# Performance work log

Hardware: AMD Instinct MI355X
Metric: run time of the kernel (lower is better)

Reference implementation:

```python
import jax, jax.numpy as jnp
import numpy as np

N_NODES = 40000
N_EDGES = 640000
N_GRAPHS = 64
D_IN = 128
D_H = 128
N_LAYERS = 3
EPS = 1e-5


def _layer_norm(x, g, b):
    mu = jnp.mean(x, axis=-1, keepdims=True)
    var = jnp.var(x, axis=-1, keepdims=True)
    return (x - mu) * jax.lax.rsqrt(var + EPS) * g + b


def _sage_conv(x, src, dst, Wl, bl, Wr):
    # mean aggregation of neighbor messages: i <- mean_{j: (j->i)} x_j
    msg = x[src]                                              # [E, d]
    agg = jax.ops.segment_sum(msg, dst, num_segments=N_NODES)  # [N, d]
    deg = jax.ops.segment_sum(jnp.ones((src.shape[0],), x.dtype), dst,
                              num_segments=N_NODES)
    agg = agg / jnp.clip(deg, 1.0)[:, None]
    # out = lin_l(agg) + lin_r(x)
    return agg @ Wl.T + bl + x @ Wr.T


def setup_inputs() -> dict:
    key = jax.random.key(0)
    ks = jax.random.split(key, 12)
    s = 0.05
    x = jax.random.normal(ks[0], (N_NODES, D_IN), jnp.float32)
    edge_index = jax.random.randint(ks[1], (2, N_EDGES), 0, N_NODES, jnp.int64)
    batch = jnp.sort(jax.random.randint(ks[2], (N_NODES,), 0, N_GRAPHS, jnp.int64))
    fc_w = jax.random.normal(ks[3], (D_H, D_IN), jnp.float32) * s
    fc_b = jax.random.normal(ks[4], (D_H,), jnp.float32) * s
    Wl = jax.random.normal(ks[5], (N_LAYERS, D_H, D_H), jnp.float32) * s
    bl = jax.random.normal(ks[6], (N_LAYERS, D_H), jnp.float32) * s
    Wr = jax.random.normal(ks[7], (N_LAYERS, D_H, D_H), jnp.float32) * s
    ln_g = jnp.ones((N_LAYERS - 1, D_H), jnp.float32)
    ln_b = jnp.zeros((N_LAYERS - 1, D_H), jnp.float32)
    return {"x": x, "edge_index": edge_index, "batch": batch,
            "fc_w": fc_w, "fc_b": fc_b, "Wl": Wl, "bl": bl, "Wr": Wr,
            "ln_g": ln_g, "ln_b": ln_b}


def reference(x, edge_index, batch, fc_w, fc_b, Wl, bl, Wr, ln_g, ln_b):
    src, dst = edge_index[0], edge_index[1]
    # input projection + ReLU
    h = jax.nn.relu(x @ fc_w.T + fc_b)
    # GraphSAGE stack: norm + ReLU between layers, none after the last
    for i in range(N_LAYERS):
        h = _sage_conv(h, src, dst, Wl[i], bl[i], Wr[i])
        if i < N_LAYERS - 1:
            h = jax.nn.relu(_layer_norm(h, ln_g[i], ln_b[i]))
    node_embed = h                                            # [N, D_H]
    graph_embed = jax.ops.segment_sum(node_embed, batch,
                                      num_segments=N_GRAPHS)  # [G, D_H]
    return node_embed, graph_embed
```

## Files before the change

kernel.cpp:

```cpp
#include <hip/hip_runtime.h>
#include <hip/hip_bf16.h>


#define N_NODES 40000
#define N_EDGES 640000
#define N_GRAPHS 64
#define D 128
#define NODE_ELEMS 5120000
#define N_TILES 1250
#define ELL_W 64
#define ZERO_INTS 48192

typedef __hip_bfloat16 bf16;
typedef __attribute__((ext_vector_type(8))) short bf16x8;
typedef __attribute__((ext_vector_type(4))) float f32x4;

__device__ __forceinline__ float b2f(bf16 v) { return __bfloat162float(v); }
__device__ __forceinline__ bf16 f2b(float v) { return __float2bfloat16(v); }
__device__ __forceinline__ float lo2f(unsigned w) { return __uint_as_float(w << 16); }
__device__ __forceinline__ float hi2f(unsigned w) { return __uint_as_float(w & 0xffff0000u); }
__device__ __forceinline__ unsigned packbf(float a, float b) {
    union { bf16 h[2]; unsigned u; } c;
    c.h[0] = f2b(a); c.h[1] = f2b(b);
    return c.u;
}
__device__ __forceinline__ int is_bf16(const unsigned* lng) {
    return (lng[0] == 0x3f803f80u) ? 1 : 0;
}
__device__ __forceinline__ int edge_is_i64(const void* edge) {
    const unsigned* ew = (const unsigned*)edge;
    return (ew[1] == 0u && ew[3] == 0u && ew[5] == 0u) ? 1 : 0;
}

union U8 { uint4 u; bf16x8 s; };

__device__ __forceinline__ bf16x8 load8(const void* base, long idx, int isb) {
    if (isb) {
        U8 t;
        t.u = *(const uint4*)((const bf16*)base + idx);
        return t.s;
    }
    const float* f = (const float*)base + idx;
    float4 f0 = *(const float4*)f;
    float4 f1 = *(const float4*)(f + 4);
    union { bf16 h[8]; bf16x8 s; } t;
    t.h[0] = f2b(f0.x); t.h[1] = f2b(f0.y); t.h[2] = f2b(f0.z); t.h[3] = f2b(f0.w);
    t.h[4] = f2b(f1.x); t.h[5] = f2b(f1.y); t.h[6] = f2b(f1.z); t.h[7] = f2b(f1.w);
    return t.s;
}

__global__ __launch_bounds__(256, 2) void k_gemm0(
    const void* __restrict__ X, const void* __restrict__ fcw,
    const void* __restrict__ fcb, bf16* __restrict__ outb,
    int* __restrict__ zbase, const unsigned* __restrict__ lngraw) {
    for (int i = blockIdx.x * 256 + threadIdx.x; i < ZERO_INTS; i += gridDim.x * 256)
        zbase[i] = 0;

    const int tid = threadIdx.x;
    const int lane = tid & 63;
    const int wave = tid >> 6;
    const int n = lane & 15, q = lane >> 4;
    const int rowgrp = wave >> 1;
    const int cb = (wave & 1) * 64;
    const int isb = is_bf16(lngraw);

    bf16x8 wf[4][4];
#pragma unroll
    for (int ct = 0; ct < 4; ct++)
#pragma unroll
        for (int ks = 0; ks < 4; ks++)
            wf[ct][ks] = load8(fcw, (long)(cb + ct * 16 + n) * 128 + ks * 32 + q * 8, isb);
    float bz[4];
#pragma unroll
    for (int ct = 0; ct < 4; ct++)
        bz[ct] = isb ? b2f(((const bf16*)fcb)[cb + ct * 16 + n])
                     : ((const float*)fcb)[cb + ct * 16 + n];

    const f32x4 zero = {0.f, 0.f, 0.f, 0.f};
    for (int tile = blockIdx.x; tile < N_TILES; tile += gridDim.x) {
        const long rbase = (long)tile * 32 + rowgrp * 16 + n;
        f32x4 acc[4] = {zero, zero, zero, zero};
        bf16x8 af[4];
#pragma unroll
        for (int ks = 0; ks < 4; ks++)
            af[ks] = load8(X, rbase * 128 + ks * 32 + q * 8, isb);
#pragma unroll
        for (int ct = 0; ct < 4; ct++)
#pragma unroll
            for (int ks = 0; ks < 4; ks++)
                acc[ct] = __builtin_amdgcn_mfma_f32_16x16x32_bf16(
                    af[ks], wf[ct][ks], acc[ct], 0, 0, 0);
#pragma unroll
        for (int ct = 0; ct < 4; ct++) {
            const int col = cb + ct * 16 + n;
#pragma unroll
            for (int r = 0; r < 4; r++) {
                const long row = (long)tile * 32 + rowgrp * 16 + q * 4 + r;
                outb[row * 128 + col] = f2b(fmaxf(acc[ct][r] + bz[ct], 0.f));
            }
        }
    }
}

#define CW2_TOTAL 99200
__global__ void k_fill(const void* __restrict__ edge, const void* __restrict__ batch,
                       const void* Wl, const void* bl, const void* Wr,
                       const void* lng, const void* lnb,
                       int* __restrict__ cursor, int* __restrict__ ell,
                       int* __restrict__ batch32, bf16* __restrict__ cw) {
    const int bid = blockIdx.x, t = threadIdx.x;
    if (bid < 2500) {
        int e = bid * 256 + t;
        int s, d;
        if (edge_is_i64(edge)) {
            s = (int)((const long long*)edge)[e];
            d = (int)((const long long*)edge)[N_EDGES + e];
        } else {
            s = ((const int*)edge)[e];
            d = ((const int*)edge)[N_EDGES + e];
        }
        int p = atomicAdd(&cursor[d], 1);
        if (p < ELL_W) ell[d * ELL_W + p] = s;
    } else if (bid < 2657) {
        int j = (bid - 2500) * 256 + t;
        if (j < N_NODES)
            batch32[j] = edge_is_i64(edge) ? (int)((const long long*)batch)[j]
                                           : ((const int*)batch)[j];
    } else {
        int i = (bid - 2657) * 256 + t;
        if (i >= CW2_TOTAL) return;
        int isb = is_bf16((const unsigned*)lng);
        const void* s; int o;
        if (i < 49152)       { s = Wl;  o = i; }
        else if (i < 49536)  { s = bl;  o = i - 49152; }
        else if (i < 98688)  { s = Wr;  o = i - 49536; }
        else if (i < 98944)  { s = lng; o = i - 98688; }
        else                 { s = lnb; o = i - 98944; }
        cw[i] = isb ? ((const bf16*)s)[o] : f2b(((const float*)s)[o]);
    }
}

__global__ void k_agg(const bf16* __restrict__ h, const int* __restrict__ cursor,
                      const int* __restrict__ ell, bf16* __restrict__ agg) {
    const int node = blockIdx.x * 16 + (threadIdx.x >> 4);
    const int l16 = threadIdx.x & 15;
    const int deg = min(cursor[node], ELL_W);
    const int dm1 = max(deg - 1, 0);
    const int* row = ell + node * ELL_W;
    const uint4* hp = (const uint4*)h;
    float a0 = 0.f, a1 = 0.f, a2 = 0.f, a3 = 0.f;
    float a4 = 0.f, a5 = 0.f, a6 = 0.f, a7 = 0.f;
    for (int e = 0; e < deg; e += 8) {
#pragma unroll
        for (int i = 0; i < 8; i++) {
            int ei = min(e + i, dm1);
            int idx = row[ei];
            uint4 w = hp[(size_t)idx * 16 + l16];
            float m = (e + i < deg) ? 1.f : 0.f;
            a0 = fmaf(m, lo2f(w.x), a0); a1 = fmaf(m, hi2f(w.x), a1);
            a2 = fmaf(m, lo2f(w.y), a2); a3 = fmaf(m, hi2f(w.y), a3);
            a4 = fmaf(m, lo2f(w.z), a4); a5 = fmaf(m, hi2f(w.z), a5);
            a6 = fmaf(m, lo2f(w.w), a6); a7 = fmaf(m, hi2f(w.w), a7);
        }
    }
    float inv = 1.f / (float)max(deg, 1);
    uint4 o;
    o.x = packbf(a0 * inv, a1 * inv);
    o.y = packbf(a2 * inv, a3 * inv);
    o.z = packbf(a4 * inv, a5 * inv);
    o.w = packbf(a6 * inv, a7 * inv);
    ((uint4*)agg)[(size_t)node * 16 + l16] = o;
}

template <int MODE>
__global__ __launch_bounds__(256, 2) void k_gemm(
    const bf16* __restrict__ A, const bf16* __restrict__ W1,
    const bf16* __restrict__ B, const bf16* __restrict__ W2,
    const bf16* __restrict__ bias, bf16* __restrict__ outb,
    void* __restrict__ outx, const bf16* __restrict__ lgam,
    const bf16* __restrict__ lbet, const unsigned* __restrict__ lngraw) {
    __shared__ float sred[2][2][16][2];
    const int tid = threadIdx.x;
    const int lane = tid & 63;
    const int wave = tid >> 6;
    const int n = lane & 15, q = lane >> 4;
    const int rowgrp = wave >> 1;
    const int cbi = wave & 1;
    const int cb = cbi * 64;
    const int isb = is_bf16(lngraw);

    bf16x8 wf[2][4][4];
#pragma unroll
    for (int p = 0; p < 2; p++) {
        const bf16* Wp = p ? W2 : W1;
#pragma unroll
        for (int ct = 0; ct < 4; ct++)
#pragma unroll
            for (int ks = 0; ks < 4; ks++) {
                U8 t;
                t.u = *(const uint4*)&Wp[(cb + ct * 16 + n) * 128 + ks * 32 + q * 8];
                wf[p][ct][ks] = t.s;
            }
    }
    float bz[4], gf[4], bf_[4];
#pragma unroll
    for (int ct = 0; ct < 4; ct++) {
        bz[ct] = b2f(bias[cb + ct * 16 + n]);
        if (MODE == 1) {
            gf[ct] = b2f(lgam[cb + ct * 16 + n]);
            bf_[ct] = b2f(lbet[cb + ct * 16 + n]);
        }
    }

    const f32x4 zero = {0.f, 0.f, 0.f, 0.f};

    for (int tile = blockIdx.x; tile < N_TILES; tile += gridDim.x) {
        const long rbase = (long)tile * 32 + rowgrp * 16 + n;
        f32x4 acc[4] = {zero, zero, zero, zero};
#pragma unroll
        for (int p = 0; p < 2; p++) {
            const bf16* Ap = p ? B : A;
            bf16x8 af[4];
#pragma unroll
            for (int ks = 0; ks < 4; ks++) {
                U8 t;
                t.u = *(const uint4*)&Ap[rbase * 128 + ks * 32 + q * 8];
                af[ks] = t.s;
            }
#pragma unroll
            for (int ct = 0; ct < 4; ct++)
#pragma unroll
                for (int ks = 0; ks < 4; ks++)
                    acc[ct] = __builtin_amdgcn_mfma_f32_16x16x32_bf16(
                        af[ks], wf[p][ct][ks], acc[ct], 0, 0, 0);
        }

        float vs[4][4];
#pragma unroll
        for (int ct = 0; ct < 4; ct++)
#pragma unroll
            for (int r = 0; r < 4; r++) vs[ct][r] = acc[ct][r] + bz[ct];

        if (MODE == 1) {
            float s[4], ss[4];
#pragma unroll
            for (int r = 0; r < 4; r++) {
                s[r] = 0.f; ss[r] = 0.f;
#pragma unroll
                for (int ct = 0; ct < 4; ct++) {
                    s[r] += vs[ct][r];
                    ss[r] += vs[ct][r] * vs[ct][r];
                }
            }
#pragma unroll
            for (int m = 1; m <= 8; m <<= 1)
#pragma unroll
                for (int r = 0; r < 4; r++) {
                    s[r] += __shfl_xor(s[r], m, 64);
                    ss[r] += __shfl_xor(ss[r], m, 64);
                }
            if (n == 0) {
#pragma unroll
                for (int r = 0; r < 4; r++) {
                    sred[rowgrp][cbi][q * 4 + r][0] = s[r];
                    sred[rowgrp][cbi][q * 4 + r][1] = ss[r];
                }
            }
            __syncthreads();
#pragma unroll
            for (int r = 0; r < 4; r++) {
                float S = s[r] + sred[rowgrp][1 - cbi][q * 4 + r][0];
                float SS = ss[r] + sred[rowgrp][1 - cbi][q * 4 + r][1];
                float mu = S * (1.f / 128.f);
                float var = SS * (1.f / 128.f) - mu * mu;
                float rstd = rsqrtf(var + 1e-5f);
#pragma unroll
                for (int ct = 0; ct < 4; ct++)
                    vs[ct][r] = fmaxf((vs[ct][r] - mu) * rstd * gf[ct] + bf_[ct], 0.f);
            }
            __syncthreads();
        }

#pragma unroll
        for (int ct = 0; ct < 4; ct++) {
            const int col = cb + ct * 16 + n;
#pragma unroll
            for (int r = 0; r < 4; r++) {
                const long row = (long)tile * 32 + rowgrp * 16 + q * 4 + r;
                float v = vs[ct][r];
                if (MODE == 1) {
                    outb[row * 128 + col] = f2b(v);
                } else {
                    if (isb) ((bf16*)outx)[row * 128 + col] = f2b(v);
                    else ((float*)outx)[row * 128 + col] = v;
                }
            }
        }
    }
}

__device__ __forceinline__ int lbound(const int* a, int n, int key) {
    int lo = 0, hi = n;
    while (lo < hi) {
        int mid = (lo + hi) >> 1;
        if (a[mid] < key) lo = mid + 1; else hi = mid;
    }
    return lo;
}

__global__ void k_graph(const void* __restrict__ node, const int* __restrict__ batch,
                        float* __restrict__ gsum, const unsigned* __restrict__ lngraw) {
    const int g = blockIdx.x >> 4, part = blockIdx.x & 15;
    const int c = threadIdx.x;
    const int isb = is_bf16(lngraw);
    const int lo = lbound(batch, N_NODES, g);
    const int hi = lbound(batch, N_NODES, g + 1);
    const int len = hi - lo;
    const int b0 = lo + (len * part) / 16;
    const int b1 = lo + (len * (part + 1)) / 16;
    float s0 = 0.f, s1 = 0.f;
    int n = b0;
    if (isb) {
        const bf16* nb = (const bf16*)node;
        for (; n + 2 <= b1; n += 2) {
            s0 += b2f(nb[(size_t)(n + 0) * 128 + c]);
            s1 += b2f(nb[(size_t)(n + 1) * 128 + c]);
        }
        for (; n < b1; n++) s0 += b2f(nb[(size_t)n * 128 + c]);
    } else {
        const float* nf = (const float*)node;
        for (; n + 2 <= b1; n += 2) {
            s0 += nf[(size_t)(n + 0) * 128 + c];
            s1 += nf[(size_t)(n + 1) * 128 + c];
        }
        for (; n < b1; n++) s0 += nf[(size_t)n * 128 + c];
    }
    atomicAdd(&gsum[g * 128 + c], s0 + s1);
}

__global__ void k_gout(const float* __restrict__ gsum, void* __restrict__ out,
                       const unsigned* __restrict__ lngraw) {
    int i = blockIdx.x * 256 + threadIdx.x;
    if (i >= N_GRAPHS * D) return;
    if (is_bf16(lngraw)) ((bf16*)out)[NODE_ELEMS + i] = f2b(gsum[i]);
    else ((float*)out)[NODE_ELEMS + i] = gsum[i];
}

extern "C" void kernel_launch(void* const* d_in, const int* in_sizes, int n_in,
                              void* d_out, int out_size, void* d_ws, size_t ws_size,
                              hipStream_t stream) {
    const void* x = d_in[0];
    const void* edge = d_in[1];
    const void* batch = d_in[2];
    const void* fc_w = d_in[3];
    const void* fc_b = d_in[4];
    const void* Wl = d_in[5];
    const void* bl = d_in[6];
    const void* Wr = d_in[7];
    const void* ln_g = d_in[8];
    const void* ln_b = d_in[9];
    const unsigned* lngraw = (const unsigned*)ln_g;

    size_t off = 0;
    char* base = (char*)d_ws;
    auto carve = [&](size_t bytes) -> char* {
        char* p = base + off;
        off = (off + bytes + 255) & ~(size_t)255;
        return p;
    };
    bf16* cw = (bf16*)carve((size_t)CW2_TOTAL * 2);
    bf16* hA = (bf16*)carve((size_t)NODE_ELEMS * 2);
    bf16* hB = (bf16*)carve((size_t)NODE_ELEMS * 2);
    bf16* agg = (bf16*)carve((size_t)NODE_ELEMS * 2);
    int* batch32 = (int*)carve((size_t)N_NODES * 4);
    int* ell = (int*)carve((size_t)N_NODES * ELL_W * 4);
    int* cursor = (int*)carve((size_t)N_NODES * 4);
    float* gsum = (float*)carve((size_t)N_GRAPHS * D * 4);

    const bf16* cw_Wl = cw;
    const bf16* cw_bl = cw + 49152;
    const bf16* cw_Wr = cw + 49536;
    const bf16* cw_lng = cw + 98688;
    const bf16* cw_lnb = cw + 98944;

    k_gemm0<<<512, 256, 0, stream>>>(x, fc_w, fc_b, hA, cursor, lngraw);
    k_fill<<<3045, 256, 0, stream>>>(edge, batch, Wl, bl, Wr, ln_g, ln_b,
                                     cursor, ell, batch32, cw);

    bf16* hcur = hA;
    bf16* hnext = hB;
    for (int l = 0; l < 3; l++) {
        k_agg<<<2500, 256, 0, stream>>>(hcur, cursor, ell, agg);
        const bf16* W1 = cw_Wl + (size_t)l * 16384;
        const bf16* W2 = cw_Wr + (size_t)l * 16384;
        const bf16* bb = cw_bl + (size_t)l * 128;
        if (l < 2) {
            k_gemm<1><<<512, 256, 0, stream>>>(agg, W1, hcur, W2, bb, hnext,
                                               nullptr, cw_lng + (size_t)l * 128,
                                               cw_lnb + (size_t)l * 128, lngraw);
            bf16* t = hcur; hcur = hnext; hnext = t;
        } else {
            k_gemm<2><<<512, 256, 0, stream>>>(agg, W1, hcur, W2, bb, nullptr,
                                               d_out, nullptr, nullptr, lngraw);
        }
    }

    k_graph<<<1024, 128, 0, stream>>>(d_out, batch32, gsum, lngraw);
    k_gout<<<32, 256, 0, stream>>>(gsum, d_out, lngraw);
}
```

Measured before the change: 265.2 us.

## Fuse input GEMM with edge bucketing and store ELL indices as uint16

Merges the input-projection GEMM kernel and the edge/batch/weight preprocessing kernel into one launch. Block roles are interleaved so MFMA GEMM tiles run alongside atomic-based ELL filling. Each edge block now handles five edges per thread. The ELL neighbor table is stored as 16-bit indices, which is valid because node ids stay below 65536; this halves its footprint and the index traffic in every aggregation pass. Cursor zeroing moves to a memset and gsum zeroing moves into the GEMM blocks, which adds a separate memset operation on the stream.

```diff
diff --git a/kernel.cpp b/kernel.cpp
--- a/kernel.cpp
+++ b/kernel.cpp
@@ -9,7 +9,6 @@
 #define NODE_ELEMS 5120000
 #define N_TILES 1250
 #define ELL_W 64
-#define ZERO_INTS 48192
 
 typedef __hip_bfloat16 bf16;
 typedef __attribute__((ext_vector_type(8))) short bf16x8;
@@ -49,85 +48,54 @@
     return t.s;
 }
 
-__global__ __launch_bounds__(256, 2) void k_gemm0(
+#define CW2_TOTAL 99200
+__global__ __launch_bounds__(256, 2) void k_main(
     const void* __restrict__ X, const void* __restrict__ fcw,
     const void* __restrict__ fcb, bf16* __restrict__ outb,
-    int* __restrict__ zbase, const unsigned* __restrict__ lngraw) {
-    for (int i = blockIdx.x * 256 + threadIdx.x; i < ZERO_INTS; i += gridDim.x * 256)
-        zbase[i] = 0;
-
-    const int tid = threadIdx.x;
-    const int lane = tid & 63;
-    const int wave = tid >> 6;
-    const int n = lane & 15, q = lane >> 4;
-    const int rowgrp = wave >> 1;
-    const int cb = (wave & 1) * 64;
-    const int isb = is_bf16(lngraw);
-
-    bf16x8 wf[4][4];
-#pragma unroll
-    for (int ct = 0; ct < 4; ct++)
-#pragma unroll
-        for (int ks = 0; ks < 4; ks++)
-            wf[ct][ks] = load8(fcw, (long)(cb + ct * 16 + n) * 128 + ks * 32 + q * 8, isb);
-    float bz[4];
-#pragma unroll
-    for (int ct = 0; ct < 4; ct++)
-        bz[ct] = isb ? b2f(((const bf16*)fcb)[cb + ct * 16 + n])
-                     : ((const float*)fcb)[cb + ct * 16 + n];
-
-    const f32x4 zero = {0.f, 0.f, 0.f, 0.f};
-    for (int tile = blockIdx.x; tile < N_TILES; tile += gridDim.x) {
-        const long rbase = (long)tile * 32 + rowgrp * 16 + n;
-        f32x4 acc[4] = {zero, zero, zero, zero};
-        bf16x8 af[4];
-#pragma unroll
-        for (int ks = 0; ks < 4; ks++)
-            af[ks] = load8(X, rbase * 128 + ks * 32 + q * 8, isb);
-#pragma unroll
-        for (int ct = 0; ct < 4; ct++)
-#pragma unroll
-            for (int ks = 0; ks < 4; ks++)
-                acc[ct] = __builtin_amdgcn_mfma_f32_16x16x32_bf16(
-                    af[ks], wf[ct][ks], acc[ct], 0, 0, 0);
-#pragma unroll
-        for (int ct = 0; ct < 4; ct++) {
-            const int col = cb + ct * 16 + n;
-#pragma unroll
-            for (int r = 0; r < 4; r++) {
-                const long row = (long)tile * 32 + rowgrp * 16 + q * 4 + r;
-                outb[row * 128 + col] = f2b(fmaxf(acc[ct][r] + bz[ct], 0.f));
-            }
-        }
-    }
-}
-
-#define CW2_TOTAL 99200
-__global__ void k_fill(const void* __restrict__ edge, const void* __restrict__ batch,
-                       const void* Wl, const void* bl, const void* Wr,
-                       const void* lng, const void* lnb,
-                       int* __restrict__ cursor, int* __restrict__ ell,
-                       int* __restrict__ batch32, bf16* __restrict__ cw) {
+    const void* __restrict__ edge, const void* __restrict__ batch,
+    const void* Wl, const void* bl, const void* Wr,
+    const void* lng, const void* lnb,
+    int* __restrict__ cursor, unsigned short* __restrict__ ell,
+    int* __restrict__ batch32, bf16* __restrict__ cw,
+    float* __restrict__ gsum) {
     const int bid = blockIdx.x, t = threadIdx.x;
-    if (bid < 2500) {
-        int e = bid * 256 + t;
-        int s, d;
-        if (edge_is_i64(edge)) {
-            s = (int)((const long long*)edge)[e];
-            d = (int)((const long long*)edge)[N_EDGES + e];
-        } else {
-            s = ((const int*)edge)[e];
-            d = ((const int*)edge)[N_EDGES + e];
-        }
-        int p = atomicAdd(&cursor[d], 1);
-        if (p < ELL_W) ell[d * ELL_W + p] = s;
-    } else if (bid < 2657) {
-        int j = (bid - 2500) * 256 + t;
+    int role, id;
+    if (bid < 1000) { role = (bid & 1) ? 0 : 1; id = bid >> 1; }
+    else if (bid < 1012) { role = 0; id = 500 + (bid - 1000); }
+    else if (bid < 1169) { role = 2; id = bid - 1012; }
+    else { role = 3; id = bid - 1169; }
+
+    if (role == 1) {
+        const int i64 = edge_is_i64(edge);
+        int s[5], d[5];
+#pragma unroll
+        for (int i = 0; i < 5; i++) {
+            int e = id * 1280 + i * 256 + t;
+            if (i64) {
+                s[i] = (int)((const long long*)edge)[e];
+                d[i] = (int)((const long long*)edge)[N_EDGES + e];
+            } else {
+                s[i] = ((const int*)edge)[e];
+                d[i] = ((const int*)edge)[N_EDGES + e];
+            }
+        }
+        int p[5];
+#pragma unroll
+        for (int i = 0; i < 5; i++) p[i] = atomicAdd(&cursor[d[i]], 1);
+#pragma unroll
+        for (int i = 0; i < 5; i++)
+            if (p[i] < ELL_W) ell[d[i] * ELL_W + p[i]] = (unsigned short)s[i];
+        return;
+    }
+    if (role == 2) {
+        int j = id * 256 + t;
         if (j < N_NODES)
             batch32[j] = edge_is_i64(edge) ? (int)((const long long*)batch)[j]
                                            : ((const int*)batch)[j];
-    } else {
-        int i = (bid - 2657) * 256 + t;
+        return;
+    }
+    if (role == 3) {
+        int i = id * 256 + t;
         if (i >= CW2_TOTAL) return;
         int isb = is_bf16((const unsigned*)lng);
         const void* s; int o;
@@ -137,16 +105,65 @@
         else if (i < 98944)  { s = lng; o = i - 98688; }
         else                 { s = lnb; o = i - 98944; }
         cw[i] = isb ? ((const bf16*)s)[o] : f2b(((const float*)s)[o]);
+        return;
+    }
+
+    {
+        int i = id * 256 + t;
+        if (i < N_GRAPHS * D) gsum[i] = 0.f;
+    }
+    const int lane = t & 63;
+    const int wave = t >> 6;
+    const int n = lane & 15, q = lane >> 4;
+    const int rowgrp = wave >> 1;
+    const int cb = (wave & 1) * 64;
+    const int isb = is_bf16((const unsigned*)lng);
+
+    bf16x8 wf[4][4];
+#pragma unroll
+    for (int ct = 0; ct < 4; ct++)
+#pragma unroll
+        for (int ks = 0; ks < 4; ks++)
+            wf[ct][ks] = load8(fcw, (long)(cb + ct * 16 + n) * 128 + ks * 32 + q * 8, isb);
+    float bz[4];
+#pragma unroll
+    for (int ct = 0; ct < 4; ct++)
+        bz[ct] = isb ? b2f(((const bf16*)fcb)[cb + ct * 16 + n])
+                     : ((const float*)fcb)[cb + ct * 16 + n];
+
+    const f32x4 zero = {0.f, 0.f, 0.f, 0.f};
+    for (int tile = id; tile < N_TILES; tile += 512) {
+        const long rbase = (long)tile * 32 + rowgrp * 16 + n;
+        f32x4 acc[4] = {zero, zero, zero, zero};
+        bf16x8 af[4];
+#pragma unroll
+        for (int ks = 0; ks < 4; ks++)
+            af[ks] = load8(X, rbase * 128 + ks * 32 + q * 8, isb);
+#pragma unroll
+        for (int ct = 0; ct < 4; ct++)
+#pragma unroll
+            for (int ks = 0; ks < 4; ks++)
+                acc[ct] = __builtin_amdgcn_mfma_f32_16x16x32_bf16(
+                    af[ks], wf[ct][ks], acc[ct], 0, 0, 0);
+#pragma unroll
+        for (int ct = 0; ct < 4; ct++) {
+            const int col = cb + ct * 16 + n;
+#pragma unroll
+            for (int r = 0; r < 4; r++) {
+                const long row = (long)tile * 32 + rowgrp * 16 + q * 4 + r;
+                outb[row * 128 + col] = f2b(fmaxf(acc[ct][r] + bz[ct], 0.f));
+            }
+        }
     }
 }
 
 __global__ void k_agg(const bf16* __restrict__ h, const int* __restrict__ cursor,
-                      const int* __restrict__ ell, bf16* __restrict__ agg) {
+                      const unsigned short* __restrict__ ell, bf16* __restrict__ agg) {
     const int node = blockIdx.x * 16 + (threadIdx.x >> 4);
     const int l16 = threadIdx.x & 15;
     const int deg = min(cursor[node], ELL_W);
     const int dm1 = max(deg - 1, 0);
-    const int* row = ell + node * ELL_W;
+    const unsigned short* row = ell + node * ELL_W;
     const uint4* hp = (const uint4*)h;
     float a0 = 0.f, a1 = 0.f, a2 = 0.f, a3 = 0.f;
     float a4 = 0.f, a5 = 0.f, a6 = 0.f, a7 = 0.f;
@@ -154,7 +171,7 @@
 #pragma unroll
         for (int i = 0; i < 8; i++) {
             int ei = min(e + i, dm1);
-            int idx = row[ei];
+            int idx = (int)row[ei];
             uint4 w = hp[(size_t)idx * 16 + l16];
             float m = (e + i < deg) ? 1.f : 0.f;
             a0 = fmaf(m, lo2f(w.x), a0); a1 = fmaf(m, hi2f(w.x), a1);
@@ -373,7 +390,7 @@
     bf16* hB = (bf16*)carve((size_t)NODE_ELEMS * 2);
     bf16* agg = (bf16*)carve((size_t)NODE_ELEMS * 2);
     int* batch32 = (int*)carve((size_t)N_NODES * 4);
-    int* ell = (int*)carve((size_t)N_NODES * ELL_W * 4);
+    unsigned short* ell = (unsigned short*)carve((size_t)N_NODES * ELL_W * 2);
     int* cursor = (int*)carve((size_t)N_NODES * 4);
     float* gsum = (float*)carve((size_t)N_GRAPHS * D * 4);
 
@@ -383,9 +400,10 @@
     const bf16* cw_lng = cw + 98688;
     const bf16* cw_lnb = cw + 98944;
 
-    k_gemm0<<<512, 256, 0, stream>>>(x, fc_w, fc_b, hA, cursor, lngraw);
-    k_fill<<<3045, 256, 0, stream>>>(edge, batch, Wl, bl, Wr, ln_g, ln_b,
-                                     cursor, ell, batch32, cw);
+    hipMemsetAsync(cursor, 0, (size_t)N_NODES * 4, stream);
+    k_main<<<1557, 256, 0, stream>>>(x, fc_w, fc_b, hA, edge, batch,
+                                     Wl, bl, Wr, ln_g, ln_b,
+                                     cursor, ell, batch32, cw, gsum);
 
     bf16* hcur = hA;
     bf16* hnext = hB;
```

After: 249.6 us. 5.9% less time.
